# Kernel tuning notes

Hardware: AMD Instinct MI355X
Metric: run time of the kernel (lower is better)

## Reference

```python
import jax, jax.numpy as jnp
import numpy as np

EMBED_SIZE = 384
HEAD_SIZE = 64

def setup_inputs() -> dict:
    key = jax.random.key(0)
    kx, kk, kq, kv = jax.random.split(key, 4)
    B, T, C = 8, 4096, EMBED_SIZE
    scale = 1.0 / np.sqrt(C)  # torch Linear default init is U(-1/sqrt(in),1/sqrt(in)); use small gaussian
    x = jax.random.normal(kx, (B, T, C), dtype=jnp.float32)
    Wk = jax.random.normal(kk, (C, HEAD_SIZE), dtype=jnp.float32) * scale  # stored as [in,out]
    Wq = jax.random.normal(kq, (C, HEAD_SIZE), dtype=jnp.float32) * scale
    Wv = jax.random.normal(kv, (C, HEAD_SIZE), dtype=jnp.float32) * scale
    return {"x": x, "Wk": Wk, "Wq": Wq, "Wv": Wv}

def reference(x, Wk, Wq, Wv):
    B, T, C = x.shape
    k = jnp.einsum('btc,ch->bth', x, Wk)
    q = jnp.einsum('btc,ch->bth', x, Wq)
    v = jnp.einsum('btc,ch->bth', x, Wv)
    # NOTE: original scales by C**0.5 (embed size), not head_size**0.5
    wei = jnp.einsum('bth,bsh->bts', q, k) / jnp.sqrt(jnp.float32(C))  # [B,T,T]
    causal = jnp.tril(jnp.ones((T, T), dtype=bool))
    wei = jnp.where(causal, wei, -jnp.inf)
    wei = jax.nn.softmax(wei, axis=-1)
    # dropout omitted (eval/deterministic mode)
    out = jnp.einsum('bts,bsh->bth', wei, v)
    return out
```

## Files before the change

kernel.cpp:

```cpp
#include <hip/hip_runtime.h>
#include <hip/hip_bf16.h>
#include <math.h>

#define EMBED 384
#define HD 64

typedef unsigned short u16;
typedef unsigned int u32;
using bf16x8 = __attribute__((ext_vector_type(8))) __bf16;
using f32x16 = __attribute__((ext_vector_type(16))) float;

__device__ inline u16 f2bf(float f) {
    union { float f; unsigned u; } v; v.f = f;
    unsigned r = v.u + 0x7fffu + ((v.u >> 16) & 1u);
    return (u16)(r >> 16);
}
__device__ inline bf16x8 ld16(const u16* p) { return *(const bf16x8*)p; }
__device__ inline u32 cvtpk(float lo, float hi) {
    u32 r;
    asm("v_cvt_pk_bf16_f32 %0, %1, %2" : "=v"(r) : "v"(lo), "v"(hi));
    return r;
}
__device__ inline void plswap(u32& a, u32& b) {
    asm volatile("v_permlane32_swap_b32 %0, %1" : "+v"(a), "+v"(b));
}

__global__ __launch_bounds__(256) void wconv(
    const float* __restrict__ Wk, const float* __restrict__ Wq,
    const float* __restrict__ Wv, u16* __restrict__ Wt)
{
    const int idx = blockIdx.x * 256 + threadIdx.x;
    if (idx >= 192 * EMBED) return;
    const int col = idx / EMBED, k = idx - col * EMBED;
    const int mat = col >> 6, c2 = col & 63;
    const float* W = (mat == 0) ? Wk : (mat == 1) ? Wq : Wv;
    float v = W[k * HD + c2];
    if (mat == 1) v *= 0.051031036307982884f * 1.4426950408889634f;
    Wt[idx] = f2bf(v);
}

#define PSTEP(kk, XA, XB, WCUR, WNXT)                                          \
  {                                                                            \
    union { u32 u[4]; bf16x8 v; } bf;                                          \
    bf.u[0] = cvtpk(XA.x, XA.y); bf.u[1] = cvtpk(XA.z, XA.w);                  \
    bf.u[2] = cvtpk(XB.x, XB.y); bf.u[3] = cvtpk(XB.z, XB.w);                  \
    if ((kk) + 1 < 24) {                                                       \
      _Pragma("unroll")                                                        \
      for (int g = 0; g < 6; ++g)                                              \
        WNXT[g] = ld16(wb + (size_t)g * 32 * EMBED + ((kk) + 1) * 16);         \
    }                                                                          \
    _Pragma("unroll")                                                          \
    for (int g = 0; g < 6; ++g)                                                \
      acc[g] = __builtin_amdgcn_mfma_f32_32x32x16_bf16(WCUR[g], bf.v, acc[g], 0, 0, 0); \
    if ((kk) + 4 < 24) {                                                       \
      XA = *(const float4*)(xr + ((kk) + 4) * 16);                             \
      XB = *(const float4*)(xr + ((kk) + 4) * 16 + 4);                         \
    }                                                                          \
  }

__global__ __launch_bounds__(64) void proj_mfma(
    const float* __restrict__ x, const u16* __restrict__ Wt,
    u16* __restrict__ kb, u16* __restrict__ qb, u16* __restrict__ vtb, int T)
{
    const int lane = threadIdx.x;
    const int c = lane & 31, h = lane >> 5;
    const int tok = blockIdx.x * 32 + c;
    const float* xr = x + (size_t)tok * EMBED + 8 * h;
    const u16* wb = Wt + (size_t)c * EMBED + 8 * h;

    f32x16 acc[6];
    #pragma unroll
    for (int g = 0; g < 6; ++g)
        #pragma unroll
        for (int r = 0; r < 16; ++r) acc[g][r] = 0.f;

    float4 x0a = *(const float4*)(xr);
    float4 x0b = *(const float4*)(xr + 4);
    float4 x1a = *(const float4*)(xr + 16);
    float4 x1b = *(const float4*)(xr + 20);
    float4 x2a = *(const float4*)(xr + 32);
    float4 x2b = *(const float4*)(xr + 36);
    float4 x3a = *(const float4*)(xr + 48);
    float4 x3b = *(const float4*)(xr + 52);

    bf16x8 wfA[6], wfB[6];
    #pragma unroll
    for (int g = 0; g < 6; ++g) wfA[g] = ld16(wb + (size_t)g * 32 * EMBED);

    for (int k4 = 0; k4 < 24; k4 += 4) {
        PSTEP(k4 + 0, x0a, x0b, wfA, wfB)
        PSTEP(k4 + 1, x1a, x1b, wfB, wfA)
        PSTEP(k4 + 2, x2a, x2b, wfA, wfB)
        PSTEP(k4 + 3, x3a, x3b, wfB, wfA)
    }

    #pragma unroll
    for (int mat = 0; mat < 2; ++mat) {
        u16* dst = (mat == 0) ? kb : qb;
        #pragma unroll
        for (int dg = 0; dg < 2; ++dg) {
            const f32x16 a = acc[mat * 2 + dg];
            #pragma unroll
            for (int k2 = 0; k2 < 4; ++k2) {
                u32 pair[2];
                pair[0] = cvtpk(a[4 * k2], a[4 * k2 + 1]);
                pair[1] = cvtpk(a[4 * k2 + 2], a[4 * k2 + 3]);
                *(uint2*)(dst + (size_t)tok * HD + dg * 32 + 8 * k2 + 4 * h) = *(uint2*)pair;
            }
        }
    }
    const int bb = tok / T, trow = tok - bb * T;
    u16* vb = vtb + (size_t)bb * HD * T + trow;
    #pragma unroll
    for (int dg = 0; dg < 2; ++dg) {
        const f32x16 a = acc[4 + dg];
        #pragma unroll
        for (int r = 0; r < 16; ++r) {
            const int dim = (r & 3) + 8 * (r >> 2) + 4 * h + 32 * dg;
            vb[(size_t)dim * T] = f2bf(a[r]);
        }
    }
}

#define LOADK(KF0, KF1, KF2, KF3, S)                                            \
  { const u16* kp_ = kbase + (size_t)(32 * (S) + c) * HD + 8 * h;               \
    KF0 = ld16(kp_); KF1 = ld16(kp_ + 16); KF2 = ld16(kp_ + 32); KF3 = ld16(kp_ + 48); }

#define COMPUTE(KF0, KF1, KF2, KF3, S)                                          \
  { const u16* vp_ = vtbase + (size_t)c * T + 32 * (S) + 8 * h;                 \
    const bf16x8 vf00 = ld16(vp_), vf01 = ld16(vp_ + 16);                       \
    const u16* vp2_ = vp_ + (size_t)32 * T;                                     \
    const bf16x8 vf10 = ld16(vp2_), vf11 = ld16(vp2_ + 16);                     \
    f32x16 st;                                                                  \
    _Pragma("unroll")                                                           \
    for (int r = 0; r < 16; ++r) st[r] = 0.f;                                   \
    __builtin_amdgcn_s_setprio(1);                                              \
    st = __builtin_amdgcn_mfma_f32_32x32x16_bf16(KF0, qf0, st, 0, 0, 0);        \
    st = __builtin_amdgcn_mfma_f32_32x32x16_bf16(KF1, qf1, st, 0, 0, 0);        \
    st = __builtin_amdgcn_mfma_f32_32x32x16_bf16(KF2, qf2, st, 0, 0, 0);        \
    st = __builtin_amdgcn_mfma_f32_32x32x16_bf16(KF3, qf3, st, 0, 0, 0);        \
    __builtin_amdgcn_s_setprio(0);                                              \
    if ((S) == q32) {                                                           \
      _Pragma("unroll")                                                         \
      for (int r = 0; r < 16; ++r) {                                            \
        const int key = (r & 3) + 8 * (r >> 2) + 4 * h;                         \
        if (key > c) st[r] = -INFINITY;                                         \
      }                                                                         \
    }                                                                           \
    float tm = fmaxf(st[0], st[1]);                                             \
    _Pragma("unroll")                                                           \
    for (int r = 2; r < 16; ++r) tm = fmaxf(tm, st[r]);                         \
    tm = fmaxf(tm, __shfl_xor(tm, 32));                                         \
    if (__any(tm > m + 11.5f)) {                                                \
      const float mn = fmaxf(m, tm);                                            \
      const float corr = exp2f(m - mn);                                         \
      m = mn;                                                                   \
      lsum *= corr;                                                             \
      _Pragma("unroll")                                                         \
      for (int r = 0; r < 16; ++r) { o0[r] *= corr; o1[r] *= corr; }            \
    }                                                                           \
    float ps = 0.f;                                                             \
    _Pragma("unroll")                                                           \
    for (int r = 0; r < 16; ++r) { st[r] = exp2f(st[r] - m); ps += st[r]; }     \
    lsum += ps + __shfl_xor(ps, 32);                                            \
    u32 w[8];                                                                   \
    _Pragma("unroll")                                                           \
    for (int q = 0; q < 8; ++q) w[q] = cvtpk(st[2 * q], st[2 * q + 1]);         \
    {                                                                           \
      u32 a0 = w[0], b0 = w[2], a1 = w[1], b1 = w[3];                           \
      plswap(a0, b0); plswap(a1, b1);                                           \
      union { u32 u[4]; bf16x8 v; } pf;                                         \
      pf.u[0] = a0; pf.u[1] = a1; pf.u[2] = b0; pf.u[3] = b1;                   \
      __builtin_amdgcn_s_setprio(1);                                            \
      o0 = __builtin_amdgcn_mfma_f32_32x32x16_bf16(vf00, pf.v, o0, 0, 0, 0);    \
      o1 = __builtin_amdgcn_mfma_f32_32x32x16_bf16(vf10, pf.v, o1, 0, 0, 0);    \
      __builtin_amdgcn_s_setprio(0);                                            \
    }                                                                           \
    {                                                                           \
      u32 a0 = w[4], b0 = w[6], a1 = w[5], b1 = w[7];                           \
      plswap(a0, b0); plswap(a1, b1);                                           \
      union { u32 u[4]; bf16x8 v; } pf;                                         \
      pf.u[0] = a0; pf.u[1] = a1; pf.u[2] = b0; pf.u[3] = b1;                   \
      __builtin_amdgcn_s_setprio(1);                                            \
      o0 = __builtin_amdgcn_mfma_f32_32x32x16_bf16(vf01, pf.v, o0, 0, 0, 0);    \
      o1 = __builtin_amdgcn_mfma_f32_32x32x16_bf16(vf11, pf.v, o1, 0, 0, 0);    \
      __builtin_amdgcn_s_setprio(0);                                            \
    }                                                                           \
  }

__global__ __launch_bounds__(256) void attn_mfma(
    const u16* __restrict__ qb, const u16* __restrict__ kb,
    const u16* __restrict__ vtb, float* __restrict__ out, int T)
{
    __shared__ float slab[4][HD][32];
    __shared__ float ml2[2][4][32];
    __shared__ float linv_s[32];

    const int b    = blockIdx.x;
    const int q32  = gridDim.y - 1 - blockIdx.y;
    const int qs   = q32 * 32;
    const int wv   = threadIdx.x >> 6;
    const int lane = threadIdx.x & 63;
    const int c = lane & 31, h = lane >> 5;

    const u16* qp = qb + ((size_t)b * T + qs + c) * HD + 8 * h;
    const bf16x8 qf0 = ld16(qp), qf1 = ld16(qp + 16);
    const bf16x8 qf2 = ld16(qp + 32), qf3 = ld16(qp + 48);

    f32x16 o0, o1;
    #pragma unroll
    for (int r = 0; r < 16; ++r) { o0[r] = 0.f; o1[r] = 0.f; }
    float m = -INFINITY, lsum = 0.f;

    const u16* kbase  = kb  + (size_t)b * T * HD;
    const u16* vtbase = vtb + (size_t)b * HD * T;

    bf16x8 kA0, kA1, kA2, kA3, kB0, kB1, kB2, kB3;
    int s = wv;
    if (s <= q32) {
        LOADK(kA0, kA1, kA2, kA3, s)
        for (;;) {
            const int sn = s + 4;
            const bool hn = sn <= q32;
            if (hn) { LOADK(kB0, kB1, kB2, kB3, sn) }
            COMPUTE(kA0, kA1, kA2, kA3, s)
            if (!hn) break;
            const int sn2 = sn + 4;
            const bool hn2 = sn2 <= q32;
            if (hn2) { LOADK(kA0, kA1, kA2, kA3, sn2) }
            COMPUTE(kB0, kB1, kB2, kB3, sn)
            if (!hn2) break;
            s = sn2;
        }
    }

    if (h == 0) { ml2[0][wv][c] = m; ml2[1][wv][c] = lsum; }
    __syncthreads();
    float M = -INFINITY;
    #pragma unroll
    for (int i = 0; i < 4; ++i) M = fmaxf(M, ml2[0][i][c]);
    float L = 0.f;
    #pragma unroll
    for (int i = 0; i < 4; ++i) L += ml2[1][i][c] * exp2f(ml2[0][i][c] - M);
    const float coef = exp2f(m - M);
    if (wv == 0 && h == 0) linv_s[c] = 1.f / L;
    #pragma unroll
    for (int r = 0; r < 16; ++r) {
        const int d0 = (r & 3) + 8 * (r >> 2) + 4 * h;
        slab[wv][d0][c]      = o0[r] * coef;
        slab[wv][d0 + 32][c] = o1[r] * coef;
    }
    __syncthreads();

    float res[8];
    #pragma unroll
    for (int j = 0; j < 8; ++j) {
        const int d = 16 * wv + 8 * h + j;
        res[j] = slab[0][d][c] + slab[1][d][c] + slab[2][d][c] + slab[3][d][c];
    }
    const float li = linv_s[c];
    float4 s0 = {res[0] * li, res[1] * li, res[2] * li, res[3] * li};
    float4 s1 = {res[4] * li, res[5] * li, res[6] * li, res[7] * li};
    float* op = out + ((size_t)b * T + qs + c) * HD + 16 * wv + 8 * h;
    *(float4*)op = s0;
    *(float4*)(op + 4) = s1;
}

extern "C" void kernel_launch(void* const* d_in, const int* in_sizes, int n_in,
                              void* d_out, int out_size, void* d_ws, size_t ws_size,
                              hipStream_t stream) {
    const float* x  = (const float*)d_in[0];
    const float* Wk = (const float*)d_in[1];
    const float* Wq = (const float*)d_in[2];
    const float* Wv = (const float*)d_in[3];
    float* out = (float*)d_out;

    const int M = in_sizes[0] / EMBED;
    const int B = 8;
    const int T = M / B;

    u16* kb  = (u16*)d_ws;
    u16* qb  = kb + (size_t)M * HD;
    u16* vtb = qb + (size_t)M * HD;
    u16* Wt  = vtb + (size_t)M * HD;

    wconv<<<(192 * EMBED + 255) / 256, 256, 0, stream>>>(Wk, Wq, Wv, Wt);
    proj_mfma<<<M / 32, 64, 0, stream>>>(x, Wt, kb, qb, vtb, T);
    dim3 g(B, T / 32);
    attn_mfma<<<g, 256, 0, stream>>>(qb, kb, vtb, out, T);
}
```

Baseline: 184.9 us.

## Repack K and V into MFMA fragment order for contiguous attention loads

Adds a repack kernel that rewrites K and transposed V into a per-32-key-block, per-lane fragment-major layout, so each wave's fragment loads in the attention loop become fully contiguous 16-byte-per-lane accesses instead of strided rows. K and V^T are staged in the output buffer as scratch before repacking. The max and sum reductions in the softmax are also rewritten as balanced trees to shorten dependency chains. The cost is an extra kernel launch and a full extra read and write of K and V.

Measured after the change: 167.5 us. 1.1x faster.

```diff
diff --git a/kernel.cpp b/kernel.cpp
--- a/kernel.cpp
+++ b/kernel.cpp
@@ -122,15 +122,38 @@
     }
 }
 
+__global__ __launch_bounds__(256) void repack(
+    const u16* __restrict__ kb, const u16* __restrict__ vtb,
+    u16* __restrict__ kfb, u16* __restrict__ vfb, int T)
+{
+    const int tid = blockIdx.x * 256 + threadIdx.x;
+    const int half = tid >> 18;
+    const int fl8 = tid & 262143;
+    const size_t fl = (size_t)fl8 * 8;
+    const int lane = fl8 & 63;
+    const int fj   = (fl8 >> 6) & 3;
+    const int bt   = fl8 >> 8;
+    const int b = bt >> 7, S = bt & 127;
+    const int c = lane & 31, h = lane >> 5;
+    if (half == 0) {
+        const u16* src = kb + ((size_t)b * T + 32 * S + c) * 64 + fj * 16 + 8 * h;
+        *(uint4*)(kfb + fl) = *(const uint4*)src;
+    } else {
+        const int dim = (fj >> 1) * 32 + c;
+        const int key = 32 * S + (fj & 1) * 16 + 8 * h;
+        const u16* src = vtb + (size_t)b * HD * T + (size_t)dim * T + key;
+        *(uint4*)(vfb + fl) = *(const uint4*)src;
+    }
+}
+
 #define LOADK(KF0, KF1, KF2, KF3, S)                                            \
-  { const u16* kp_ = kbase + (size_t)(32 * (S) + c) * HD + 8 * h;               \
-    KF0 = ld16(kp_); KF1 = ld16(kp_ + 16); KF2 = ld16(kp_ + 32); KF3 = ld16(kp_ + 48); }
+  { const u16* kp_ = kbase2 + (size_t)(S) * 2048 + lane8;                       \
+    KF0 = ld16(kp_); KF1 = ld16(kp_ + 512); KF2 = ld16(kp_ + 1024); KF3 = ld16(kp_ + 1536); }
 
 #define COMPUTE(KF0, KF1, KF2, KF3, S)                                          \
-  { const u16* vp_ = vtbase + (size_t)c * T + 32 * (S) + 8 * h;                 \
-    const bf16x8 vf00 = ld16(vp_), vf01 = ld16(vp_ + 16);                       \
-    const u16* vp2_ = vp_ + (size_t)32 * T;                                     \
-    const bf16x8 vf10 = ld16(vp2_), vf11 = ld16(vp2_ + 16);                     \
+  { const u16* vp_ = vbase2 + (size_t)(S) * 2048 + lane8;                       \
+    const bf16x8 vf00 = ld16(vp_),        vf01 = ld16(vp_ + 512);               \
+    const bf16x8 vf10 = ld16(vp_ + 1024), vf11 = ld16(vp_ + 1536);              \
     f32x16 st;                                                                  \
     _Pragma("unroll")                                                           \
     for (int r = 0; r < 16; ++r) st[r] = 0.f;                                   \
@@ -147,9 +170,13 @@
         if (key > c) st[r] = -INFINITY;                                         \
       }                                                                         \
     }                                                                           \
-    float tm = fmaxf(st[0], st[1]);                                             \
-    _Pragma("unroll")                                                           \
-    for (int r = 2; r < 16; ++r) tm = fmaxf(tm, st[r]);                         \
+    float tm;                                                                   \
+    { float a0 = fmaxf(st[0], st[1]),  a1 = fmaxf(st[2], st[3]);                \
+      float a2 = fmaxf(st[4], st[5]),  a3 = fmaxf(st[6], st[7]);                \
+      float a4 = fmaxf(st[8], st[9]),  a5 = fmaxf(st[10], st[11]);              \
+      float a6 = fmaxf(st[12], st[13]), a7 = fmaxf(st[14], st[15]);             \
+      a0 = fmaxf(a0, a1); a2 = fmaxf(a2, a3); a4 = fmaxf(a4, a5); a6 = fmaxf(a6, a7); \
+      tm = fmaxf(fmaxf(a0, a2), fmaxf(a4, a6)); }                               \
     tm = fmaxf(tm, __shfl_xor(tm, 32));                                         \
     if (__any(tm > m + 11.5f)) {                                                \
       const float mn = fmaxf(m, tm);                                            \
@@ -159,9 +186,15 @@
       _Pragma("unroll")                                                         \
       for (int r = 0; r < 16; ++r) { o0[r] *= corr; o1[r] *= corr; }            \
     }                                                                           \
-    float ps = 0.f;                                                             \
     _Pragma("unroll")                                                           \
-    for (int r = 0; r < 16; ++r) { st[r] = exp2f(st[r] - m); ps += st[r]; }     \
+    for (int r = 0; r < 16; ++r) st[r] = exp2f(st[r] - m);                      \
+    float ps;                                                                   \
+    { float a0 = st[0] + st[1],  a1 = st[2] + st[3];                            \
+      float a2 = st[4] + st[5],  a3 = st[6] + st[7];                            \
+      float a4 = st[8] + st[9],  a5 = st[10] + st[11];                          \
+      float a6 = st[12] + st[13], a7 = st[14] + st[15];                         \
+      a0 += a1; a2 += a3; a4 += a5; a6 += a7;                                   \
+      ps = (a0 + a2) + (a4 + a6); }                                             \
     lsum += ps + __shfl_xor(ps, 32);                                            \
     u32 w[8];                                                                   \
     _Pragma("unroll")                                                           \
@@ -189,8 +222,8 @@
   }
 
 __global__ __launch_bounds__(256) void attn_mfma(
-    const u16* __restrict__ qb, const u16* __restrict__ kb,
-    const u16* __restrict__ vtb, float* __restrict__ out, int T)
+    const u16* __restrict__ qb, const u16* __restrict__ kfb,
+    const u16* __restrict__ vfb, float* __restrict__ out, int T)
 {
     __shared__ float slab[4][HD][32];
     __shared__ float ml2[2][4][32];
@@ -202,6 +235,7 @@
     const int wv   = threadIdx.x >> 6;
     const int lane = threadIdx.x & 63;
     const int c = lane & 31, h = lane >> 5;
+    const int lane8 = lane * 8;
 
     const u16* qp = qb + ((size_t)b * T + qs + c) * HD + 8 * h;
     const bf16x8 qf0 = ld16(qp), qf1 = ld16(qp + 16);
@@ -212,8 +246,8 @@
     for (int r = 0; r < 16; ++r) { o0[r] = 0.f; o1[r] = 0.f; }
     float m = -INFINITY, lsum = 0.f;
 
-    const u16* kbase  = kb  + (size_t)b * T * HD;
-    const u16* vtbase = vtb + (size_t)b * HD * T;
+    const u16* kbase2 = kfb + (size_t)b * T * HD;
+    const u16* vbase2 = vfb + (size_t)b * T * HD;
 
     bf16x8 kA0, kA1, kA2, kA3, kB0, kB1, kB2, kB3;
     int s = wv;
@@ -279,13 +313,16 @@
     const int B = 8;
     const int T = M / B;
 
-    u16* kb  = (u16*)d_ws;
-    u16* qb  = kb + (size_t)M * HD;
-    u16* vtb = qb + (size_t)M * HD;
-    u16* Wt  = vtb + (size_t)M * HD;
+    u16* kfb = (u16*)d_ws;
+    u16* qb  = kfb + (size_t)M * HD;
+    u16* vfb = qb + (size_t)M * HD;
+    u16* Wt  = vfb + (size_t)M * HD;
+    u16* kb  = (u16*)d_out;
+    u16* vtb = kb + (size_t)M * HD;
 
     wconv<<<(192 * EMBED + 255) / 256, 256, 0, stream>>>(Wk, Wq, Wv, Wt);
     proj_mfma<<<M / 32, 64, 0, stream>>>(x, Wt, kb, qb, vtb, T);
+    repack<<<2048, 256, 0, stream>>>(kb, vtb, kfb, vfb, T);
     dim3 g(B, T / 32);
-    attn_mfma<<<g, 256, 0, stream>>>(qb, kb, vtb, out, T);
-}
+    attn_mfma<<<g, 256, 0, stream>>>(qb, kfb, vfb, out, T);
+}
```
